# Performance work log

Measured on AMD Instinct MI355X. Metric: run time of the kernel, lower is better.

The kernel has to match this reference:

```python
import jax, jax.numpy as jnp
import numpy as np

HEAD_DIM = 256
NUM_HEADS = 8
NUM_KV_HEADS = 1
ROPE_BASE = 10000.0
NEG_INF = -1e9


def _rope_cos_sin(position_ids):
    # inv_freq: [head_dim/2]
    inv_freq = 1.0 / (ROPE_BASE ** (jnp.arange(0, HEAD_DIM, 2, dtype=jnp.float32) / HEAD_DIM))
    # freqs: [B, S, head_dim/2]
    freqs = position_ids.astype(jnp.float32)[:, :, None] * inv_freq[None, None, :]
    emb = jnp.concatenate([freqs, freqs], axis=-1)  # [B, S, head_dim]
    return jnp.cos(emb), jnp.sin(emb)


def _rotate_half(x):
    x1, x2 = x[..., : HEAD_DIM // 2], x[..., HEAD_DIM // 2 :]
    return jnp.concatenate([-x2, x1], axis=-1)


def setup_inputs() -> dict:
    key = jax.random.key(0)
    ks = jax.random.split(key, 5)
    B, S, D = 2, 2048, 2048
    hidden_states = jax.random.normal(ks[0], (B, S, D), dtype=jnp.float32)
    # additive causal mask: 0 on/below diagonal, -1e9 above
    causal = jnp.triu(jnp.full((S, S), NEG_INF, dtype=jnp.float32), k=1)
    attention_mask = jnp.broadcast_to(causal[None, None], (B, 1, S, S))
    position_ids = jnp.broadcast_to(jnp.arange(S, dtype=jnp.int64 if jax.config.jax_enable_x64 else jnp.int32)[None], (B, S))
    Wq = jax.random.normal(ks[1], (NUM_HEADS * HEAD_DIM, D), dtype=jnp.float32) * 0.02
    Wk = jax.random.normal(ks[2], (NUM_KV_HEADS * HEAD_DIM, D), dtype=jnp.float32) * 0.02
    Wv = jax.random.normal(ks[3], (NUM_KV_HEADS * HEAD_DIM, D), dtype=jnp.float32) * 0.02
    Wo = jax.random.normal(ks[4], (D, NUM_HEADS * HEAD_DIM), dtype=jnp.float32) * 0.02
    return {"hidden_states": hidden_states, "attention_mask": attention_mask,
            "position_ids": position_ids, "Wq": Wq, "Wk": Wk, "Wv": Wv, "Wo": Wo}


def reference(hidden_states, attention_mask, position_ids, Wq, Wk, Wv, Wo):
    B, S, D = hidden_states.shape
    n_rep = NUM_HEADS // NUM_KV_HEADS
    # projections (no bias)
    q = (hidden_states @ Wq.T).reshape(B, S, NUM_HEADS, HEAD_DIM).transpose(0, 2, 1, 3)
    k = (hidden_states @ Wk.T).reshape(B, S, NUM_KV_HEADS, HEAD_DIM).transpose(0, 2, 1, 3)
    v = (hidden_states @ Wv.T).reshape(B, S, NUM_KV_HEADS, HEAD_DIM).transpose(0, 2, 1, 3)
    # rotary embeddings, broadcast over heads (unsqueeze_dim=1)
    cos, sin = _rope_cos_sin(position_ids)  # [B, S, head_dim]
    cos, sin = cos[:, None], sin[:, None]
    q = q * cos + _rotate_half(q) * sin
    k = k * cos + _rotate_half(k) * sin
    # repeat_kv: expand kv heads to match query heads
    k = jnp.repeat(k, n_rep, axis=1)  # [B, H, S, Dh]
    v = jnp.repeat(v, n_rep, axis=1)
    scores = jnp.einsum('bhqd,bhkd->bhqk', q, k) / jnp.sqrt(jnp.float32(HEAD_DIM))
    scores = scores + attention_mask
    attn_weights = jax.nn.softmax(scores.astype(jnp.float32), axis=-1).astype(q.dtype)
    attn_output = jnp.einsum('bhqk,bhkd->bhqd', attn_weights, v)
    attn_output = attn_output.transpose(0, 2, 1, 3).reshape(B, S, NUM_HEADS * HEAD_DIM)
    attn_output = attn_output @ Wo.T
    return attn_output, attn_weights
```

## Files before the change

### kernel.cpp

```cpp
#include <hip/hip_runtime.h>
#include <math.h>

#define SEQ 2048
#define DM  2048
#define NH  8
#define HD  256
#define NB  2

typedef __attribute__((ext_vector_type(8))) short bf16x8;
typedef __attribute__((ext_vector_type(4))) float f32x4;

__device__ inline short f2b(float f) {
    union { float f; unsigned u; } x; x.f = f;
    unsigned r = x.u + 0x7fffu + ((x.u >> 16) & 1u);
    return (short)(r >> 16);
}
__device__ inline float b2f(short s) {
    union { unsigned u; float f; } x;
    x.u = ((unsigned)(unsigned short)s) << 16;
    return x.f;
}

typedef unsigned int u32_g __attribute__((address_space(1)));
typedef unsigned int u32_l __attribute__((address_space(3)));
__device__ inline void gl2lds(const void* g, void* l) {
    __builtin_amdgcn_global_load_lds((const u32_g*)g, (u32_l*)l, 16, 0, 0);
}

__global__ void convert_all(const float* __restrict__ hs, const float* __restrict__ wq,
                            const float* __restrict__ wk, const float* __restrict__ wv,
                            const float* __restrict__ wo,
                            short* __restrict__ hsb, short* __restrict__ wcat,
                            short* __restrict__ wob)
{
    int i4 = blockIdx.x * 256 + threadIdx.x;
    const float* src; short* dst; int s4, d4;
    if (i4 < 2097152)      { src = hs; dst = hsb;  s4 = i4;           d4 = s4; }
    else if (i4 < 3145728) { src = wq; dst = wcat; s4 = i4 - 2097152; d4 = s4; }
    else if (i4 < 3276800) { src = wk; dst = wcat; s4 = i4 - 3145728; d4 = 1048576 + s4; }
    else if (i4 < 3407872) { src = wv; dst = wcat; s4 = i4 - 3276800; d4 = 1179648 + s4; }
    else                   { src = wo; dst = wob;  s4 = i4 - 3407872; d4 = s4; }
    float4 v = ((const float4*)src)[s4];
    short4 o;
    o.x = f2b(v.x); o.y = f2b(v.y); o.z = f2b(v.z); o.w = f2b(v.w);
    ((short4*)dst)[d4] = o;
}

template<int MODE>
__global__ __launch_bounds__(256, 2) void gemm_bt(const short* __restrict__ A,
                                                  const short* __restrict__ Bw,
                                                  float* __restrict__ C,
                                                  short* __restrict__ q_o,
                                                  short* __restrict__ k_o,
                                                  short* __restrict__ v_o,
                                                  int M, int N, int K)
{
    __shared__ short As[128 * 32];
    __shared__ short Bs[128 * 32];
    int tid = threadIdx.x;
    int lane = tid & 63, w = tid >> 6;
    int lm = lane & 15, quad = lane >> 4;
    int wm = w & 1, wn = w >> 1;
    int m0 = blockIdx.y * 128, n0 = blockIdx.x * 128;

    f32x4 acc[16];
#pragma unroll
    for (int i = 0; i < 16; ++i) acc[i] = (f32x4){0.f, 0.f, 0.f, 0.f};

    const char* Aptr = (const char*)A + (size_t)m0 * K * 2;
    const char* Bptr = (const char*)Bw + (size_t)n0 * K * 2;

    for (int k0 = 0; k0 < K; k0 += 32) {
#pragma unroll
        for (int it = 0; it < 2; ++it) {
            int f = it * 4096 + tid * 16;
            int row = f >> 6, colb = f & 63;
            gl2lds(Aptr + (size_t)row * (K * 2) + k0 * 2 + colb, (char*)As + f);
            gl2lds(Bptr + (size_t)row * (K * 2) + k0 * 2 + colb, (char*)Bs + f);
        }
        __syncthreads();
        bf16x8 af[4], bfr[4];
#pragma unroll
        for (int mt = 0; mt < 4; ++mt)
            af[mt] = *(const bf16x8*)(As + (wm * 64 + mt * 16 + lm) * 32 + quad * 8);
#pragma unroll
        for (int nt = 0; nt < 4; ++nt)
            bfr[nt] = *(const bf16x8*)(Bs + (wn * 64 + nt * 16 + lm) * 32 + quad * 8);
#pragma unroll
        for (int mt = 0; mt < 4; ++mt)
#pragma unroll
            for (int nt = 0; nt < 4; ++nt)
                acc[mt * 4 + nt] = __builtin_amdgcn_mfma_f32_16x16x32_bf16(
                    af[mt], bfr[nt], acc[mt * 4 + nt], 0, 0, 0);
        __syncthreads();
    }

#pragma unroll
    for (int mt = 0; mt < 4; ++mt)
#pragma unroll
        for (int nt = 0; nt < 4; ++nt) {
            f32x4 a = acc[mt * 4 + nt];
            int col = n0 + wn * 64 + nt * 16 + lm;
#pragma unroll
            for (int i = 0; i < 4; ++i) {
                int m = m0 + wm * 64 + mt * 16 + quad * 4 + i;
                if (MODE == 0) {
                    C[(size_t)m * N + col] = a[i];
                } else {
                    int b = m >> 11, s = m & (SEQ - 1);
                    short hv = f2b(a[i]);
                    if (col < DM) {
                        int hh = col >> 8, d = col & (HD - 1);
                        q_o[(((size_t)(b * NH + hh)) * SEQ + s) * HD + d] = hv;
                    } else if (col < DM + HD) {
                        int d = col - DM;
                        int c2 = (d >> 3) ^ (s & 31);
                        k_o[((size_t)b * SEQ + s) * HD + (c2 << 3) + (d & 7)] = hv;
                    } else {
                        int d = col - DM - HD;
                        int sc = ((s >> 3) & 7) ^ (d & 7);
                        v_o[((size_t)(b * HD + d)) * SEQ + (s & ~63) + (sc << 3) + (s & 7)] = hv;
                    }
                }
            }
        }
}

__global__ void rope_kernel(short* __restrict__ q, short* __restrict__ k,
                            const int* __restrict__ pos)
{
    const int QP = NB * NH * SEQ * 128;
    const int KP = NB * SEQ * 128;
    const float C0 = 0.07195578415606394f;
    const float R2PI = 0.15915494309189535f;
    int idx = blockIdx.x * 256 + threadIdx.x;
    if (idx < QP) {
        int d = idx & 127;
        int s = (idx >> 7) & (SEQ - 1);
        int h = (idx >> 18) & (NH - 1);
        int b = idx >> 21;
        float p = (float)pos[b * SEQ + s];
        float fr = p * __expf(-(float)d * C0);
        float rv = fr * R2PI; rv -= floorf(rv);
        float c = __builtin_amdgcn_cosf(rv), sn = __builtin_amdgcn_sinf(rv);
        size_t base = (((size_t)(b * NH + h)) * SEQ + s) * HD + d;
        float x0 = b2f(q[base]), x1 = b2f(q[base + 128]);
        q[base]       = f2b(x0 * c - x1 * sn);
        q[base + 128] = f2b(x1 * c + x0 * sn);
    } else {
        int j = idx - QP;
        if (j < KP) {
            int d = j & 127;
            int s = (j >> 7) & (SEQ - 1);
            int b = j >> 18;
            float p = (float)pos[b * SEQ + s];
            float fr = p * __expf(-(float)d * C0);
            float rv = fr * R2PI; rv -= floorf(rv);
            float c = __builtin_amdgcn_cosf(rv), sn = __builtin_amdgcn_sinf(rv);
            int e0 = ((((d >> 3) ^ (s & 31)) & 31) << 3) | (d & 7);
            size_t base = ((size_t)(b * SEQ + s)) * HD;
            float x0 = b2f(k[base + e0]), x1 = b2f(k[base + (e0 ^ 128)]);
            k[base + e0]         = f2b(x0 * c - x1 * sn);
            k[base + (e0 ^ 128)] = f2b(x1 * c + x0 * sn);
        }
    }
}

__global__ __launch_bounds__(256, 2) void attn_flash(const short* __restrict__ qb,
                                                     const short* __restrict__ kb,
                                                     const short* __restrict__ vT,
                                                     float* __restrict__ w_out,
                                                     short* __restrict__ a_o)
{
    __shared__ short Ks[64 * 256];
    __shared__ short Vs[256 * 64];
    __shared__ short P[4][16][72];

    int tid = threadIdx.x;
    int w = tid >> 6, lane = tid & 63;
    int lm = lane & 15, quad = lane >> 4;
    int idx = blockIdx.x;
    int hb = idx & 15;
    int h = hb & 7, b = hb >> 3;
    int tq = (idx < 256) ? (31 - (idx >> 4)) : ((idx - 256) >> 4);
    int q0 = tq * 64;
    int r0 = q0 + w * 16;

    const short* qrow = qb + (((size_t)(b * NH + h)) * SEQ + r0 + lm) * HD;
    bf16x8 qf[8];
#pragma unroll
    for (int ks = 0; ks < 8; ++ks)
        qf[ks] = *(const bf16x8*)(qrow + ks * 32 + quad * 8);

    float m_r[4], l_r[4];
    f32x4 O[16];
#pragma unroll
    for (int i = 0; i < 4; ++i) { m_r[i] = -INFINITY; l_r[i] = 0.f; }
#pragma unroll
    for (int i = 0; i < 16; ++i) O[i] = (f32x4){0.f, 0.f, 0.f, 0.f};

    const short* kb0 = kb + (size_t)b * SEQ * HD;
    const short* vb0 = vT + (size_t)b * HD * SEQ;

    f32x4 kreg[8], vreg[8];

    auto issue_kv = [&](int t) {
        const short* kt = kb0 + (size_t)t * 64 * HD;
        const short* vt = vb0 + (size_t)t * 64;
#pragma unroll
        for (int it = 0; it < 8; ++it) {
            int g = it * 256 + tid;
            kreg[it] = *(const f32x4*)(kt + (g >> 5) * HD + (g & 31) * 8);
            vreg[it] = *(const f32x4*)(vt + (size_t)(g >> 3) * SEQ + (g & 7) * 8);
        }
    };
    auto issue_k = [&](int t) {
        const short* kt = kb0 + (size_t)t * 64 * HD;
#pragma unroll
        for (int it = 0; it < 8; ++it) {
            int g = it * 256 + tid;
            kreg[it] = *(const f32x4*)(kt + (g >> 5) * HD + (g & 31) * 8);
        }
    };

    issue_kv(0);

    for (int tk = 0; tk <= tq; ++tk) {
#pragma unroll
        for (int it = 0; it < 8; ++it) {
            int g = it * 256 + tid;
            *(f32x4*)((char*)Ks + g * 16) = kreg[it];
            *(f32x4*)((char*)Vs + g * 16) = vreg[it];
        }
        __syncthreads();
        if (tk < tq) issue_kv(tk + 1);

        f32x4 sa[4];
#pragma unroll
        for (int nt = 0; nt < 4; ++nt) sa[nt] = (f32x4){0.f, 0.f, 0.f, 0.f};
        __builtin_amdgcn_s_setprio(1);
#pragma unroll
        for (int ks = 0; ks < 8; ++ks)
#pragma unroll
            for (int nt = 0; nt < 4; ++nt) {
                int s_l = nt * 16 + lm;
                bf16x8 kf = *(const bf16x8*)(Ks + s_l * 256 +
                                             (((ks * 4 + quad) ^ (s_l & 31)) << 3));
                sa[nt] = __builtin_amdgcn_mfma_f32_16x16x32_bf16(qf[ks], kf, sa[nt], 0, 0, 0);
            }
        __builtin_amdgcn_s_setprio(0);

        float vals[4][4];
#pragma unroll
        for (int nt = 0; nt < 4; ++nt)
#pragma unroll
            for (int i = 0; i < 4; ++i) {
                float v = sa[nt][i] * 0.0625f;
                if (tk == tq && (nt * 16 + lm) > (w * 16 + quad * 4 + i)) v -= 1e9f;
                vals[nt][i] = v;
            }
        float mnew[4], alpha[4], ps[4];
#pragma unroll
        for (int i = 0; i < 4; ++i) {
            float mx = fmaxf(fmaxf(vals[0][i], vals[1][i]), fmaxf(vals[2][i], vals[3][i]));
            mx = fmaxf(mx, __shfl_xor(mx, 1));
            mx = fmaxf(mx, __shfl_xor(mx, 2));
            mx = fmaxf(mx, __shfl_xor(mx, 4));
            mx = fmaxf(mx, __shfl_xor(mx, 8));
            mnew[i] = fmaxf(m_r[i], mx);
            alpha[i] = __expf(m_r[i] - mnew[i]);
            ps[i] = 0.f;
        }
#pragma unroll
        for (int nt = 0; nt < 4; ++nt)
#pragma unroll
            for (int i = 0; i < 4; ++i) {
                float p = __expf(vals[nt][i] - mnew[i]);
                ps[i] += p;
                P[w][quad * 4 + i][nt * 16 + lm] = f2b(p);
            }
        f32x4 al;
#pragma unroll
        for (int i = 0; i < 4; ++i) {
            float t = ps[i];
            t += __shfl_xor(t, 1); t += __shfl_xor(t, 2);
            t += __shfl_xor(t, 4); t += __shfl_xor(t, 8);
            l_r[i] = l_r[i] * alpha[i] + t;
            m_r[i] = mnew[i];
            al[i] = alpha[i];
        }
#pragma unroll
        for (int nt2 = 0; nt2 < 16; ++nt2) O[nt2] *= al;

        const short* prow = &P[w][lm][0];
        __builtin_amdgcn_s_setprio(1);
#pragma unroll
        for (int kc = 0; kc < 2; ++kc) {
            bf16x8 pf = *(const bf16x8*)(prow + kc * 32 + quad * 8);
#pragma unroll
            for (int nt2 = 0; nt2 < 16; ++nt2) {
                int d_l = nt2 * 16 + lm;
                bf16x8 vf = *(const bf16x8*)(Vs + d_l * 64 +
                                             (((kc * 4 + quad) ^ (d_l & 7)) << 3));
                O[nt2] = __builtin_amdgcn_mfma_f32_16x16x32_bf16(pf, vf, O[nt2], 0, 0, 0);
            }
        }
        __builtin_amdgcn_s_setprio(0);
        __syncthreads();
    }

    f32x4 li;
#pragma unroll
    for (int i = 0; i < 4; ++i) li[i] = 1.f / l_r[i];

    issue_k(0);

#pragma unroll
    for (int nt2 = 0; nt2 < 16; ++nt2)
#pragma unroll
        for (int i = 0; i < 4; ++i) {
            size_t s = (size_t)q0 + w * 16 + quad * 4 + i;
            a_o[((size_t)b * SEQ + s) * DM + h * HD + nt2 * 16 + lm] = f2b(O[nt2][i] * li[i]);
        }

    float* wb = w_out + (((size_t)(b * NH + h)) * SEQ) * SEQ;
    for (int tk = 0; tk <= tq; ++tk) {
#pragma unroll
        for (int it = 0; it < 8; ++it) {
            int g = it * 256 + tid;
            *(f32x4*)((char*)Ks + g * 16) = kreg[it];
        }
        __syncthreads();
        if (tk < tq) issue_k(tk + 1);

        f32x4 sa[4];
#pragma unroll
        for (int nt = 0; nt < 4; ++nt) sa[nt] = (f32x4){0.f, 0.f, 0.f, 0.f};
        __builtin_amdgcn_s_setprio(1);
#pragma unroll
        for (int ks = 0; ks < 8; ++ks)
#pragma unroll
            for (int nt = 0; nt < 4; ++nt) {
                int s_l = nt * 16 + lm;
                bf16x8 kf = *(const bf16x8*)(Ks + s_l * 256 +
                                             (((ks * 4 + quad) ^ (s_l & 31)) << 3));
                sa[nt] = __builtin_amdgcn_mfma_f32_16x16x32_bf16(qf[ks], kf, sa[nt], 0, 0, 0);
            }
        __builtin_amdgcn_s_setprio(0);
#pragma unroll
        for (int nt = 0; nt < 4; ++nt)
#pragma unroll
            for (int i = 0; i < 4; ++i) {
                float v = sa[nt][i] * 0.0625f;
                if (tk == tq && (nt * 16 + lm) > (w * 16 + quad * 4 + i)) v -= 1e9f;
                float wv = __expf(v - m_r[i]) * li[i];
                __builtin_nontemporal_store(
                    wv, wb + (size_t)(r0 + quad * 4 + i) * SEQ + tk * 64 + nt * 16 + lm);
            }
        __syncthreads();
    }

    int zs = (tq + 1) * 64;
    if (zs < SEQ) {
        int r = tid >> 2, c0 = (tid & 3) * 4;
        float* wr = wb + (size_t)(q0 + r) * SEQ;
        f32x4 z = (f32x4){0.f, 0.f, 0.f, 0.f};
        for (int c = zs + c0; c < SEQ; c += 16)
            __builtin_nontemporal_store(z, (f32x4*)(wr + c));
    }
}

extern "C" void kernel_launch(void* const* d_in, const int* in_sizes, int n_in,
                              void* d_out, int out_size, void* d_ws, size_t ws_size,
                              hipStream_t stream)
{
    const float* hs   = (const float*)d_in[0];
    const int*   pos  = (const int*)d_in[2];
    const float* Wq   = (const float*)d_in[3];
    const float* Wk   = (const float*)d_in[4];
    const float* Wv   = (const float*)d_in[5];
    const float* Wo   = (const float*)d_in[6];

    float* out      = (float*)d_out;
    float* attn_out = out;
    float* w_out    = out + (size_t)NB * SEQ * DM;

    short* hsb  = (short*)d_ws;
    short* a_b  = hsb;
    short* wcat = hsb + 8388608;
    short* wob  = wcat + 5242880;
    short* qx   = wob + 4194304;
    short* kx   = qx + 8388608;
    short* vTx  = kx + 1048576;

    convert_all<<<17408, 256, 0, stream>>>(hs, Wq, Wk, Wv, Wo, hsb, wcat, wob);
    gemm_bt<1><<<dim3(20, 32), 256, 0, stream>>>(hsb, wcat, nullptr, qx, kx, vTx,
                                                 NB * SEQ, DM + 2 * HD, DM);
    rope_kernel<<<18432, 256, 0, stream>>>(qx, kx, pos);
    attn_flash<<<512, 256, 0, stream>>>(qx, kx, vTx, w_out, a_b);
    gemm_bt<0><<<dim3(16, 32), 256, 0, stream>>>(a_b, wob, attn_out, nullptr, nullptr, nullptr,
                                                 NB * SEQ, DM, DM);
}
```

Baseline: 622.7 us.

## Pair complementary causal query tiles per block with double-buffered direct-to-LDS K/V staging

Each 512-thread block now handles two query tiles, a short one and a long one, so they share K/V tile loads and the causal work per block is balanced. K/V staging switches from register round-trips to global-to-LDS direct loads into double-buffered shared memory, with one waitcnt and barrier per iteration. Nontemporal stores for the weights and zero-fill are replaced with regular stores. LDS use per block doubles (about 130KB), which may limit residency to one block per CU, and the short-tile half of the block sits idle while the long tile finishes.

```diff
diff --git a/kernel.cpp b/kernel.cpp
--- a/kernel.cpp
+++ b/kernel.cpp
@@ -166,25 +166,29 @@
     }
 }
 
-__global__ __launch_bounds__(256, 2) void attn_flash(const short* __restrict__ qb,
+__global__ __launch_bounds__(512, 2) void attn_flash(const short* __restrict__ qb,
                                                      const short* __restrict__ kb,
                                                      const short* __restrict__ vT,
                                                      float* __restrict__ w_out,
                                                      short* __restrict__ a_o)
 {
-    __shared__ short Ks[64 * 256];
-    __shared__ short Vs[256 * 64];
-    __shared__ short P[4][16][72];
+    __shared__ short Ks[2][64 * 256];
+    __shared__ short Vs[2][256 * 64];
+    __shared__ short P[8][16][72];
 
     int tid = threadIdx.x;
     int w = tid >> 6, lane = tid & 63;
     int lm = lane & 15, quad = lane >> 4;
+    int wl = w & 3;
+    int grp = w >> 2;
     int idx = blockIdx.x;
     int hb = idx & 15;
     int h = hb & 7, b = hb >> 3;
-    int tq = (idx < 256) ? (31 - (idx >> 4)) : ((idx - 256) >> 4);
+    int p = idx >> 4;
+    int tq = grp ? (31 - p) : p;
+    int tmax = 31 - p;
     int q0 = tq * 64;
-    int r0 = q0 + w * 16;
+    int r0 = q0 + wl * 16;
 
     const short* qrow = qb + (((size_t)(b * NH + h)) * SEQ + r0 + lm) * HD;
     bf16x8 qf[8];
@@ -202,171 +206,172 @@
     const short* kb0 = kb + (size_t)b * SEQ * HD;
     const short* vb0 = vT + (size_t)b * HD * SEQ;
 
-    f32x4 kreg[8], vreg[8];
-
-    auto issue_kv = [&](int t) {
-        const short* kt = kb0 + (size_t)t * 64 * HD;
-        const short* vt = vb0 + (size_t)t * 64;
-#pragma unroll
-        for (int it = 0; it < 8; ++it) {
-            int g = it * 256 + tid;
-            kreg[it] = *(const f32x4*)(kt + (g >> 5) * HD + (g & 31) * 8);
-            vreg[it] = *(const f32x4*)(vt + (size_t)(g >> 3) * SEQ + (g & 7) * 8);
+    auto STAGE_KV = [&](int t, int bi) {
+        const char* kt = (const char*)(kb0 + (size_t)t * 64 * HD);
+#pragma unroll
+        for (int it = 0; it < 4; ++it) {
+            int g = it * 512 + tid;
+            gl2lds(kt + ((size_t)(g >> 5) * HD + (g & 31) * 8) * 2, (char*)Ks[bi] + g * 16);
+            gl2lds((const char*)vb0 + ((size_t)(g >> 3) * SEQ + t * 64 + (g & 7) * 8) * 2,
+                   (char*)Vs[bi] + g * 16);
         }
     };
-    auto issue_k = [&](int t) {
-        const short* kt = kb0 + (size_t)t * 64 * HD;
-#pragma unroll
-        for (int it = 0; it < 8; ++it) {
-            int g = it * 256 + tid;
-            kreg[it] = *(const f32x4*)(kt + (g >> 5) * HD + (g & 31) * 8);
+    auto STAGE_K = [&](int t, int bi) {
+        const char* kt = (const char*)(kb0 + (size_t)t * 64 * HD);
+#pragma unroll
+        for (int it = 0; it < 4; ++it) {
+            int g = it * 512 + tid;
+            gl2lds(kt + ((size_t)(g >> 5) * HD + (g & 31) * 8) * 2, (char*)Ks[bi] + g * 16);
         }
     };
 
-    issue_kv(0);
-
-    for (int tk = 0; tk <= tq; ++tk) {
-#pragma unroll
-        for (int it = 0; it < 8; ++it) {
-            int g = it * 256 + tid;
-            *(f32x4*)((char*)Ks + g * 16) = kreg[it];
-            *(f32x4*)((char*)Vs + g * 16) = vreg[it];
-        }
-        __syncthreads();
-        if (tk < tq) issue_kv(tk + 1);
-
-        f32x4 sa[4];
-#pragma unroll
-        for (int nt = 0; nt < 4; ++nt) sa[nt] = (f32x4){0.f, 0.f, 0.f, 0.f};
-        __builtin_amdgcn_s_setprio(1);
-#pragma unroll
-        for (int ks = 0; ks < 8; ++ks)
-#pragma unroll
-            for (int nt = 0; nt < 4; ++nt) {
-                int s_l = nt * 16 + lm;
-                bf16x8 kf = *(const bf16x8*)(Ks + s_l * 256 +
-                                             (((ks * 4 + quad) ^ (s_l & 31)) << 3));
-                sa[nt] = __builtin_amdgcn_mfma_f32_16x16x32_bf16(qf[ks], kf, sa[nt], 0, 0, 0);
+    STAGE_KV(0, 0);
+    asm volatile("s_waitcnt vmcnt(0)" ::: "memory");
+    __syncthreads();
+
+    int cur = 0;
+    for (int tk = 0; tk <= tmax; ++tk) {
+        if (tk < tmax) STAGE_KV(tk + 1, cur ^ 1);
+
+        if (tk <= tq) {
+            f32x4 sa[4];
+#pragma unroll
+            for (int nt = 0; nt < 4; ++nt) sa[nt] = (f32x4){0.f, 0.f, 0.f, 0.f};
+            __builtin_amdgcn_s_setprio(1);
+#pragma unroll
+            for (int ks = 0; ks < 8; ++ks)
+#pragma unroll
+                for (int nt = 0; nt < 4; ++nt) {
+                    int s_l = nt * 16 + lm;
+                    bf16x8 kf = *(const bf16x8*)(Ks[cur] + s_l * 256 +
+                                                 (((ks * 4 + quad) ^ (s_l & 31)) << 3));
+                    sa[nt] = __builtin_amdgcn_mfma_f32_16x16x32_bf16(qf[ks], kf, sa[nt], 0, 0, 0);
+                }
+            __builtin_amdgcn_s_setprio(0);
+
+            float vals[4][4];
+#pragma unroll
+            for (int nt = 0; nt < 4; ++nt)
+#pragma unroll
+                for (int i = 0; i < 4; ++i) {
+                    float v = sa[nt][i] * 0.0625f;
+                    if (tk == tq && (nt * 16 + lm) > (wl * 16 + quad * 4 + i)) v -= 1e9f;
+                    vals[nt][i] = v;
+                }
+            float mnew[4], alpha[4], ps[4];
+#pragma unroll
+            for (int i = 0; i < 4; ++i) {
+                float mx = fmaxf(fmaxf(vals[0][i], vals[1][i]), fmaxf(vals[2][i], vals[3][i]));
+                mx = fmaxf(mx, __shfl_xor(mx, 1));
+                mx = fmaxf(mx, __shfl_xor(mx, 2));
+                mx = fmaxf(mx, __shfl_xor(mx, 4));
+                mx = fmaxf(mx, __shfl_xor(mx, 8));
+                mnew[i] = fmaxf(m_r[i], mx);
+                alpha[i] = __expf(m_r[i] - mnew[i]);
+                ps[i] = 0.f;
             }
-        __builtin_amdgcn_s_setprio(0);
-
-        float vals[4][4];
-#pragma unroll
-        for (int nt = 0; nt < 4; ++nt)
+#pragma unroll
+            for (int nt = 0; nt < 4; ++nt)
+#pragma unroll
+                for (int i = 0; i < 4; ++i) {
+                    float pp = __expf(vals[nt][i] - mnew[i]);
+                    ps[i] += pp;
+                    P[w][quad * 4 + i][nt * 16 + lm] = f2b(pp);
+                }
+            f32x4 al;
 #pragma unroll
             for (int i = 0; i < 4; ++i) {
-                float v = sa[nt][i] * 0.0625f;
-                if (tk == tq && (nt * 16 + lm) > (w * 16 + quad * 4 + i)) v -= 1e9f;
-                vals[nt][i] = v;
+                float t = ps[i];
+                t += __shfl_xor(t, 1); t += __shfl_xor(t, 2);
+                t += __shfl_xor(t, 4); t += __shfl_xor(t, 8);
+                l_r[i] = l_r[i] * alpha[i] + t;
+                m_r[i] = mnew[i];
+                al[i] = alpha[i];
             }
-        float mnew[4], alpha[4], ps[4];
+#pragma unroll
+            for (int nt2 = 0; nt2 < 16; ++nt2) O[nt2] *= al;
+
+            const short* prow = &P[w][lm][0];
+            __builtin_amdgcn_s_setprio(1);
+#pragma unroll
+            for (int kc = 0; kc < 2; ++kc) {
+                bf16x8 pf = *(const bf16x8*)(prow + kc * 32 + quad * 8);
+#pragma unroll
+                for (int nt2 = 0; nt2 < 16; ++nt2) {
+                    int d_l = nt2 * 16 + lm;
+                    bf16x8 vf = *(const bf16x8*)(Vs[cur] + d_l * 64 +
+                                                 (((kc * 4 + quad) ^ (d_l & 7)) << 3));
+                    O[nt2] = __builtin_amdgcn_mfma_f32_16x16x32_bf16(pf, vf, O[nt2], 0, 0, 0);
+                }
+            }
+            __builtin_amdgcn_s_setprio(0);
+        }
+
+        asm volatile("s_waitcnt vmcnt(0)" ::: "memory");
+        __builtin_amdgcn_s_barrier();
+        cur ^= 1;
+    }
+
+    f32x4 li;
+#pragma unroll
+    for (int i = 0; i < 4; ++i) li[i] = 1.f / l_r[i];
+
+#pragma unroll
+    for (int nt2 = 0; nt2 < 16; ++nt2)
 #pragma unroll
         for (int i = 0; i < 4; ++i) {
-            float mx = fmaxf(fmaxf(vals[0][i], vals[1][i]), fmaxf(vals[2][i], vals[3][i]));
-            mx = fmaxf(mx, __shfl_xor(mx, 1));
-            mx = fmaxf(mx, __shfl_xor(mx, 2));
-            mx = fmaxf(mx, __shfl_xor(mx, 4));
-            mx = fmaxf(mx, __shfl_xor(mx, 8));
-            mnew[i] = fmaxf(m_r[i], mx);
-            alpha[i] = __expf(m_r[i] - mnew[i]);
-            ps[i] = 0.f;
-        }
-#pragma unroll
-        for (int nt = 0; nt < 4; ++nt)
-#pragma unroll
-            for (int i = 0; i < 4; ++i) {
-                float p = __expf(vals[nt][i] - mnew[i]);
-                ps[i] += p;
-                P[w][quad * 4 + i][nt * 16 + lm] = f2b(p);
-            }
-        f32x4 al;
-#pragma unroll
-        for (int i = 0; i < 4; ++i) {
-            float t = ps[i];
-            t += __shfl_xor(t, 1); t += __shfl_xor(t, 2);
-            t += __shfl_xor(t, 4); t += __shfl_xor(t, 8);
-            l_r[i] = l_r[i] * alpha[i] + t;
-            m_r[i] = mnew[i];
-            al[i] = alpha[i];
-        }
-#pragma unroll
-        for (int nt2 = 0; nt2 < 16; ++nt2) O[nt2] *= al;
-
-        const short* prow = &P[w][lm][0];
-        __builtin_amdgcn_s_setprio(1);
-#pragma unroll
-        for (int kc = 0; kc < 2; ++kc) {
-            bf16x8 pf = *(const bf16x8*)(prow + kc * 32 + quad * 8);
-#pragma unroll
-            for (int nt2 = 0; nt2 < 16; ++nt2) {
-                int d_l = nt2 * 16 + lm;
-                bf16x8 vf = *(const bf16x8*)(Vs + d_l * 64 +
-                                             (((kc * 4 + quad) ^ (d_l & 7)) << 3));
-                O[nt2] = __builtin_amdgcn_mfma_f32_16x16x32_bf16(pf, vf, O[nt2], 0, 0, 0);
-            }
-        }
-        __builtin_amdgcn_s_setprio(0);
-        __syncthreads();
-    }
-
-    f32x4 li;
-#pragma unroll
-    for (int i = 0; i < 4; ++i) li[i] = 1.f / l_r[i];
-
-    issue_k(0);
-
-#pragma unroll
-    for (int nt2 = 0; nt2 < 16; ++nt2)
-#pragma unroll
-        for (int i = 0; i < 4; ++i) {
-            size_t s = (size_t)q0 + w * 16 + quad * 4 + i;
+            size_t s = (size_t)q0 + wl * 16 + quad * 4 + i;
             a_o[((size_t)b * SEQ + s) * DM + h * HD + nt2 * 16 + lm] = f2b(O[nt2][i] * li[i]);
         }
 
+    STAGE_K(0, 0);
+    asm volatile("s_waitcnt vmcnt(0)" ::: "memory");
+    __syncthreads();
+
     float* wb = w_out + (((size_t)(b * NH + h)) * SEQ) * SEQ;
-    for (int tk = 0; tk <= tq; ++tk) {
-#pragma unroll
-        for (int it = 0; it < 8; ++it) {
-            int g = it * 256 + tid;
-            *(f32x4*)((char*)Ks + g * 16) = kreg[it];
-        }
-        __syncthreads();
-        if (tk < tq) issue_k(tk + 1);
-
-        f32x4 sa[4];
-#pragma unroll
-        for (int nt = 0; nt < 4; ++nt) sa[nt] = (f32x4){0.f, 0.f, 0.f, 0.f};
-        __builtin_amdgcn_s_setprio(1);
-#pragma unroll
-        for (int ks = 0; ks < 8; ++ks)
-#pragma unroll
-            for (int nt = 0; nt < 4; ++nt) {
-                int s_l = nt * 16 + lm;
-                bf16x8 kf = *(const bf16x8*)(Ks + s_l * 256 +
-                                             (((ks * 4 + quad) ^ (s_l & 31)) << 3));
-                sa[nt] = __builtin_amdgcn_mfma_f32_16x16x32_bf16(qf[ks], kf, sa[nt], 0, 0, 0);
-            }
-        __builtin_amdgcn_s_setprio(0);
-#pragma unroll
-        for (int nt = 0; nt < 4; ++nt)
-#pragma unroll
-            for (int i = 0; i < 4; ++i) {
-                float v = sa[nt][i] * 0.0625f;
-                if (tk == tq && (nt * 16 + lm) > (w * 16 + quad * 4 + i)) v -= 1e9f;
-                float wv = __expf(v - m_r[i]) * li[i];
-                __builtin_nontemporal_store(
-                    wv, wb + (size_t)(r0 + quad * 4 + i) * SEQ + tk * 64 + nt * 16 + lm);
-            }
-        __syncthreads();
+    cur = 0;
+    for (int tk = 0; tk <= tmax; ++tk) {
+        if (tk < tmax) STAGE_K(tk + 1, cur ^ 1);
+
+        if (tk <= tq) {
+            f32x4 sa[4];
+#pragma unroll
+            for (int nt = 0; nt < 4; ++nt) sa[nt] = (f32x4){0.f, 0.f, 0.f, 0.f};
+            __builtin_amdgcn_s_setprio(1);
+#pragma unroll
+            for (int ks = 0; ks < 8; ++ks)
+#pragma unroll
+                for (int nt = 0; nt < 4; ++nt) {
+                    int s_l = nt * 16 + lm;
+                    bf16x8 kf = *(const bf16x8*)(Ks[cur] + s_l * 256 +
+                                                 (((ks * 4 + quad) ^ (s_l & 31)) << 3));
+                    sa[nt] = __builtin_amdgcn_mfma_f32_16x16x32_bf16(qf[ks], kf, sa[nt], 0, 0, 0);
+                }
+            __builtin_amdgcn_s_setprio(0);
+#pragma unroll
+            for (int nt = 0; nt < 4; ++nt)
+#pragma unroll
+                for (int i = 0; i < 4; ++i) {
+                    float v = sa[nt][i] * 0.0625f;
+                    if (tk == tq && (nt * 16 + lm) > (wl * 16 + quad * 4 + i)) v -= 1e9f;
+                    float wv = __expf(v - m_r[i]) * li[i];
+                    wb[(size_t)(r0 + quad * 4 + i) * SEQ + tk * 64 + nt * 16 + lm] = wv;
+                }
+        }
+
+        asm volatile("s_waitcnt vmcnt(0)" ::: "memory");
+        __builtin_amdgcn_s_barrier();
+        cur ^= 1;
     }
 
     int zs = (tq + 1) * 64;
     if (zs < SEQ) {
-        int r = tid >> 2, c0 = (tid & 3) * 4;
+        int tg = tid & 255;
+        int r = tg >> 2, c0 = (tg & 3) * 4;
         float* wr = wb + (size_t)(q0 + r) * SEQ;
         f32x4 z = (f32x4){0.f, 0.f, 0.f, 0.f};
         for (int c = zs + c0; c < SEQ; c += 16)
-            __builtin_nontemporal_store(z, (f32x4*)(wr + c));
+            *(f32x4*)(wr + c) = z;
     }
 }
 
@@ -397,7 +402,7 @@
     gemm_bt<1><<<dim3(20, 32), 256, 0, stream>>>(hsb, wcat, nullptr, qx, kx, vTx,
                                                  NB * SEQ, DM + 2 * HD, DM);
     rope_kernel<<<18432, 256, 0, stream>>>(qx, kx, pos);
-    attn_flash<<<512, 256, 0, stream>>>(qx, kx, vTx, w_out, a_b);
+    attn_flash<<<256, 512, 0, stream>>>(qx, kx, vTx, w_out, a_b);
     gemm_bt<0><<<dim3(16, 32), 256, 0, stream>>>(a_b, wob, attn_out, nullptr, nullptr, nullptr,
                                                  NB * SEQ, DM, DM);
 }
```

Result: no change. 618.7 us (-0.6%).
